# Optimization experiments

Hardware: AMD Instinct MI355X
Metric: run time of the kernel (lower is better)

Reference implementation:

```python
import jax, jax.numpy as jnp
import numpy as np

N, C, K = 262144, 64, 27  # active voxels, channels, 3^3 kernel offsets


def setup_inputs() -> dict:
    key = jax.random.key(0)
    k1, k2, k3, k4, k5, k6, k7 = jax.random.split(key, 7)
    features = jax.random.normal(k1, (N, C), dtype=jnp.float32)
    # kernel map: for each offset k and output voxel n, index of contributing input voxel
    nbr_idx = jax.random.randint(k2, (K, N), 0, N, dtype=jnp.int32)
    mask = jax.random.uniform(k3, (K, N)) < 0.4
    scale = 1.0 / np.sqrt(K * C)
    w1 = jax.random.normal(k4, (K, C, C), dtype=jnp.float32) * scale
    b1 = jax.random.normal(k5, (C,), dtype=jnp.float32) * 0.01
    w2 = jax.random.normal(k6, (K, C, C), dtype=jnp.float32) * scale
    b2 = jax.random.normal(k7, (C,), dtype=jnp.float32) * 0.01
    return dict(features=features, nbr_idx=nbr_idx, mask=mask,
                w1=w1, b1=b1, w2=w2, b2=b2)


def _sparse_conv(feat, nbr_idx, mask, W, b):
    """Explicit-GEMM sparse conv: per kernel offset, gather -> GEMM -> accumulate."""
    def step(acc, xs):
        idx, m, Wk = xs                                  # [N], [N], [C, C]
        g = feat[idx] * m[:, None].astype(feat.dtype)    # gather + zero invalid: [N, C]
        return acc + g @ Wk, None
    acc, _ = jax.lax.scan(step, jnp.zeros_like(feat), (nbr_idx, mask, W))
    return acc + b


def reference(features, nbr_idx, mask, w1, b1, w2, b2):
    h = _sparse_conv(features, nbr_idx, mask, w1, b1)
    h = _sparse_conv(h, nbr_idx, mask, w2, b2)
    return h + features  # residual add of input feature tensor
```

## Files before the change

kernel.cpp:

```cpp
#include <hip/hip_runtime.h>
#include <stdint.h>

#define N_VOX 262144
#define CCH 64
#define KOFF 27

typedef short v8s __attribute__((ext_vector_type(8)));
typedef float v4f __attribute__((ext_vector_type(4)));

#define GLD16(gp, lp) __builtin_amdgcn_global_load_lds(                     \
    (const __attribute__((address_space(1))) void*)(gp),                    \
    (__attribute__((address_space(3))) void*)(lp), 16, 0, 0)

__device__ __forceinline__ unsigned short f2bf(float f) {
  unsigned u = __float_as_uint(f);
  u += 0x7fff + ((u >> 16) & 1);
  return (unsigned short)(u >> 16);
}

__global__ void prep_flag_k(const unsigned* __restrict__ m, int* __restrict__ flag) {
  if (threadIdx.x == 0) {
    int wordlike = 1;
    for (int i = 0; i < 256; ++i) {
      unsigned v = m[i];
      if (v > 1u && v != 0x3f800000u) { wordlike = 0; break; }
    }
    *flag = wordlike ? 0 : 2;
  }
}

__global__ void prep_mask_k(const void* __restrict__ m, const int* __restrict__ flag,
                            unsigned char* __restrict__ mb, int n) {
  int f = *flag;
  for (int i = blockIdx.x * blockDim.x + threadIdx.x; i < n; i += gridDim.x * blockDim.x) {
    unsigned char v;
    if (f == 2) v = (((const unsigned char*)m)[i] != 0);
    else        v = (((const unsigned*)m)[i] != 0u);
    mb[i] = v;
  }
}

__global__ void prep_feat_k(const float* __restrict__ src, unsigned short* __restrict__ dst, int n8) {
  int i = blockIdx.x * blockDim.x + threadIdx.x;
  if (i >= n8) return;
  const float4* s4 = (const float4*)src;
  float4 a = s4[i * 2], b = s4[i * 2 + 1];
  v8s v;
  v[0] = (short)f2bf(a.x); v[1] = (short)f2bf(a.y);
  v[2] = (short)f2bf(a.z); v[3] = (short)f2bf(a.w);
  v[4] = (short)f2bf(b.x); v[5] = (short)f2bf(b.y);
  v[6] = (short)f2bf(b.z); v[7] = (short)f2bf(b.w);
  ((v8s*)dst)[i] = v;
}

__global__ void prep_w_k(const float* __restrict__ w, unsigned short* __restrict__ wt) {
  int i = blockIdx.x * blockDim.x + threadIdx.x;
  if (i >= KOFF * CCH * CCH) return;
  int e = i & 7, lane = (i >> 3) & 63, ch = (i >> 9) & 7, k = i >> 12;
  int ct = ch >> 1, half = ch & 1;
  int col = ct * 16 + (lane & 15);
  int kk = half * 32 + ((lane >> 4) << 3) + e;
  wt[i] = f2bf(w[(k << 12) + (kk << 6) + col]);
}

__device__ __forceinline__ void conv_body(
    int k, bool last, char* slot, const v8s* __restrict__ Wc, char* WnB,
    const char* __restrict__ src8B, const char* __restrict__ wfgB,
    const int* __restrict__ nbr, const unsigned char* __restrict__ mb,
    int lane, int g, int tid16, int r0, int r1,
    int& jz0, int& jz1, int& mz0, int& mz1,
    int jd0, int jd1, int md0, int md1,
    v4f (&acc)[2][4])
{
  asm volatile("s_waitcnt vmcnt(4)" ::: "memory");
  v8s a0 = *(const v8s*)(slot + lane * 16);
  v8s a1 = *(const v8s*)(slot + 1024 + lane * 16);
  v8s a2 = *(const v8s*)(slot + 2048 + lane * 16);
  v8s a3 = *(const v8s*)(slot + 3072 + lane * 16);
  if (!mz0) { a0 = (v8s){}; a1 = (v8s){}; }
  if (!mz1) { a2 = (v8s){}; a3 = (v8s){}; }
  asm volatile("s_waitcnt lgkmcnt(0)" ::: "memory");
  __builtin_amdgcn_sched_barrier(0);

  if (!last) {
    GLD16(wfgB + (size_t)(k + 1) * 8192 + tid16, WnB);
    long e0 = (long)(md0 ? jd0 : 0) * 128 + g * 16;
    long e1 = (long)(md1 ? jd1 : 0) * 128 + g * 16;
    GLD16(src8B + e0,      slot);
    GLD16(src8B + e0 + 64, slot + 1024);
    GLD16(src8B + e1,      slot + 2048);
    GLD16(src8B + e1 + 64, slot + 3072);
    const int kj = (k + 2 < KOFF) ? k + 2 : KOFF - 1;
    jz0 = nbr[kj * N_VOX + r0]; jz1 = nbr[kj * N_VOX + r1];
    mz0 = mb[kj * N_VOX + r0];  mz1 = mb[kj * N_VOX + r1];
  }

#pragma unroll
  for (int ct = 0; ct < 4; ++ct) {
    v8s blo = Wc[ct * 128 + lane];
    v8s bhi = Wc[ct * 128 + 64 + lane];
    acc[0][ct] = __builtin_amdgcn_mfma_f32_16x16x32_bf16(a0, blo, acc[0][ct], 0, 0, 0);
    acc[0][ct] = __builtin_amdgcn_mfma_f32_16x16x32_bf16(a1, bhi, acc[0][ct], 0, 0, 0);
    acc[1][ct] = __builtin_amdgcn_mfma_f32_16x16x32_bf16(a2, blo, acc[1][ct], 0, 0, 0);
    acc[1][ct] = __builtin_amdgcn_mfma_f32_16x16x32_bf16(a3, bhi, acc[1][ct], 0, 0, 0);
  }

  if (!last) {
    asm volatile("s_waitcnt vmcnt(8)" ::: "memory");
    __builtin_amdgcn_s_barrier();
  }
}

template <int LAYER>
__global__ __launch_bounds__(512, 4)
void conv_layer_k(const char* __restrict__ src8B, const int* __restrict__ nbr,
                  const unsigned char* __restrict__ mb,
                  const char* __restrict__ wfgB, const float* __restrict__ bias,
                  const float* __restrict__ resid, void* __restrict__ outp) {
  __shared__ char ldsW[2][8192];
  __shared__ char ldsA[8][4096];
  const int tid = threadIdx.x;
  const int lane = tid & 63;
  const int wv = tid >> 6;
  const int l15 = lane & 15;
  const int g = lane >> 4;
  const int tid16 = tid * 16;
  const int rowbase = blockIdx.x * 256 + wv * 32;
  const int r0 = rowbase + l15;
  const int r1 = r0 + 16;
  char* slot = ldsA[wv];

  int jE0 = nbr[r0], jE1 = nbr[r1];
  int mE0 = mb[r0],  mE1 = mb[r1];
  {
    long e0 = (long)(mE0 ? jE0 : 0) * 128 + g * 16;
    long e1 = (long)(mE1 ? jE1 : 0) * 128 + g * 16;
    GLD16(src8B + e0,      slot);
    GLD16(src8B + e0 + 64, slot + 1024);
    GLD16(src8B + e1,      slot + 2048);
    GLD16(src8B + e1 + 64, slot + 3072);
  }
  GLD16(wfgB + tid16, (char*)ldsW[0] + wv * 1024);
  int jO0 = nbr[N_VOX + r0], jO1 = nbr[N_VOX + r1];
  int mO0 = mb[N_VOX + r0],  mO1 = mb[N_VOX + r1];
  asm volatile("s_waitcnt vmcnt(0)" ::: "memory");
  __builtin_amdgcn_s_barrier();

  v4f acc[2][4] = {};

#pragma unroll 1
  for (int k = 0; k < KOFF - 1; k += 2) {
    conv_body(k, false, slot, (const v8s*)ldsW[0], (char*)ldsW[1] + wv * 1024,
              src8B, wfgB, nbr, mb, lane, g, tid16, r0, r1,
              jE0, jE1, mE0, mE1, jO0, jO1, mO0, mO1, acc);
    conv_body(k + 1, false, slot, (const v8s*)ldsW[1], (char*)ldsW[0] + wv * 1024,
              src8B, wfgB, nbr, mb, lane, g, tid16, r0, r1,
              jO0, jO1, mO0, mO1, jE0, jE1, mE0, mE1, acc);
  }
  conv_body(KOFF - 1, true, slot, (const v8s*)ldsW[0], (char*)ldsW[1] + wv * 1024,
            src8B, wfgB, nbr, mb, lane, g, tid16, r0, r1,
            jE0, jE1, mE0, mE1, jO0, jO1, mO0, mO1, acc);

  float bv[4];
#pragma unroll
  for (int ct = 0; ct < 4; ++ct) bv[ct] = bias[ct * 16 + l15];

#pragma unroll
  for (int rt = 0; rt < 2; ++rt) {
    int row0 = rowbase + rt * 16 + g * 4;
#pragma unroll
    for (int ct = 0; ct < 4; ++ct) {
      int col = ct * 16 + l15;
#pragma unroll
      for (int i = 0; i < 4; ++i) {
        float v = acc[rt][ct][i] + bv[ct];
        int o = (row0 + i) * CCH + col;
        if (LAYER == 1) ((unsigned short*)outp)[o] = f2bf(v);
        else            ((float*)outp)[o] = v + resid[o];
      }
    }
  }
}

extern "C" void kernel_launch(void* const* d_in, const int* in_sizes, int n_in,
                              void* d_out, int out_size, void* d_ws, size_t ws_size,
                              hipStream_t stream) {
  const float* feat = (const float*)d_in[0];
  const int* nbr    = (const int*)d_in[1];
  const void* mask  = d_in[2];
  const float* w1   = (const float*)d_in[3];
  const float* b1   = (const float*)d_in[4];
  const float* w2   = (const float*)d_in[5];
  const float* b2   = (const float*)d_in[6];

  char* ws = (char*)d_ws;
  unsigned short* featb = (unsigned short*)ws;
  unsigned short* hb    = (unsigned short*)(ws + 33554432);
  unsigned char*  maskb = (unsigned char*)(ws + 67108864);
  unsigned short* wf1   = (unsigned short*)(ws + 74186752);
  unsigned short* wf2   = (unsigned short*)(ws + 74407936);
  int*            flag  = (int*)(ws + 74629120);

  prep_flag_k<<<1, 64, 0, stream>>>((const unsigned*)mask, flag);
  prep_mask_k<<<4096, 256, 0, stream>>>(mask, flag, maskb, KOFF * N_VOX);
  prep_feat_k<<<8192, 256, 0, stream>>>(feat, featb, N_VOX * CCH / 8);
  prep_w_k<<<432, 256, 0, stream>>>(w1, wf1);
  prep_w_k<<<432, 256, 0, stream>>>(w2, wf2);

  conv_layer_k<1><<<1024, 512, 0, stream>>>((const char*)featb, nbr, maskb,
                                            (const char*)wf1, b1, nullptr, (void*)hb);
  conv_layer_k<2><<<1024, 512, 0, stream>>>((const char*)hb, nbr, maskb,
                                            (const char*)wf2, b2, feat, (void*)d_out);
}
```

Measured before the change: 250.3 us.

## Double-buffer gathered rows, stage weights through registers, halve block size

```diff
diff --git a/kernel.cpp b/kernel.cpp
--- a/kernel.cpp
+++ b/kernel.cpp
@@ -64,41 +64,47 @@
 }
 
 __device__ __forceinline__ void conv_body(
-    int k, bool last, char* slot, const v8s* __restrict__ Wc, char* WnB,
-    const char* __restrict__ src8B, const char* __restrict__ wfgB,
+    int k, bool last, char* Wb, char* slotC, char* slotN,
+    const char* __restrict__ src8B, const v8s* __restrict__ wfg,
     const int* __restrict__ nbr, const unsigned char* __restrict__ mb,
-    int lane, int g, int tid16, int r0, int r1,
-    int& jz0, int& jz1, int& mz0, int& mz1,
-    int jd0, int jd1, int md0, int md1,
+    int lane, int wv, int g, int l15, int rme,
+    int& iN, int& mN, int& mc0, int& mc1,
     v4f (&acc)[2][4])
 {
-  asm volatile("s_waitcnt vmcnt(4)" ::: "memory");
-  v8s a0 = *(const v8s*)(slot + lane * 16);
-  v8s a1 = *(const v8s*)(slot + 1024 + lane * 16);
-  v8s a2 = *(const v8s*)(slot + 2048 + lane * 16);
-  v8s a3 = *(const v8s*)(slot + 3072 + lane * 16);
-  if (!mz0) { a0 = (v8s){}; a1 = (v8s){}; }
-  if (!mz1) { a2 = (v8s){}; a3 = (v8s){}; }
-  asm volatile("s_waitcnt lgkmcnt(0)" ::: "memory");
-  __builtin_amdgcn_sched_barrier(0);
-
+  asm volatile("s_waitcnt vmcnt(2)" ::: "memory");
+  v8s w0, w1;
+  int v0 = 0, v1 = 0;
   if (!last) {
-    GLD16(wfgB + (size_t)(k + 1) * 8192 + tid16, WnB);
-    long e0 = (long)(md0 ? jd0 : 0) * 128 + g * 16;
-    long e1 = (long)(md1 ? jd1 : 0) * 128 + g * 16;
-    GLD16(src8B + e0,      slot);
-    GLD16(src8B + e0 + 64, slot + 1024);
-    GLD16(src8B + e1,      slot + 2048);
-    GLD16(src8B + e1 + 64, slot + 3072);
+    w0 = wfg[(k + 1) * 512 + wv * 128 + lane];
+    w1 = wfg[(k + 1) * 512 + wv * 128 + 64 + lane];
+    asm volatile("s_waitcnt vmcnt(2)" ::: "memory");
+    int j0 = __shfl(iN, l15, 64);
+    int j1 = __shfl(iN, 16 + l15, 64);
+    v0 = __shfl(mN, l15, 64);
+    v1 = __shfl(mN, 16 + l15, 64);
+    long e0 = (long)(v0 ? j0 : 0) * 128 + g * 16;
+    long e1 = (long)(v1 ? j1 : 0) * 128 + g * 16;
+    GLD16(src8B + e0,      slotN);
+    GLD16(src8B + e0 + 64, slotN + 1024);
+    GLD16(src8B + e1,      slotN + 2048);
+    GLD16(src8B + e1 + 64, slotN + 3072);
     const int kj = (k + 2 < KOFF) ? k + 2 : KOFF - 1;
-    jz0 = nbr[kj * N_VOX + r0]; jz1 = nbr[kj * N_VOX + r1];
-    mz0 = mb[kj * N_VOX + r0];  mz1 = mb[kj * N_VOX + r1];
-  }
+    iN = nbr[kj * N_VOX + rme];
+    mN = mb[kj * N_VOX + rme];
+  }
+
+  v8s a0 = *(const v8s*)(slotC + lane * 16);
+  v8s a1 = *(const v8s*)(slotC + 1024 + lane * 16);
+  v8s a2 = *(const v8s*)(slotC + 2048 + lane * 16);
+  v8s a3 = *(const v8s*)(slotC + 3072 + lane * 16);
+  if (!mc0) { a0 = (v8s){}; a1 = (v8s){}; }
+  if (!mc1) { a2 = (v8s){}; a3 = (v8s){}; }
+  mc0 = v0; mc1 = v1;
 
 #pragma unroll
   for (int ct = 0; ct < 4; ++ct) {
-    v8s blo = Wc[ct * 128 + lane];
-    v8s bhi = Wc[ct * 128 + 64 + lane];
+    v8s blo = *(const v8s*)(Wb + (ct * 2) * 1024 + lane * 16);
+    v8s bhi = *(const v8s*)(Wb + (ct * 2 + 1) * 1024 + lane * 16);
     acc[0][ct] = __builtin_amdgcn_mfma_f32_16x16x32_bf16(a0, blo, acc[0][ct], 0, 0, 0);
     acc[0][ct] = __builtin_amdgcn_mfma_f32_16x16x32_bf16(a1, bhi, acc[0][ct], 0, 0, 0);
     acc[1][ct] = __builtin_amdgcn_mfma_f32_16x16x32_bf16(a2, blo, acc[1][ct], 0, 0, 0);
@@ -106,60 +112,70 @@
   }
 
   if (!last) {
-    asm volatile("s_waitcnt vmcnt(8)" ::: "memory");
+    asm volatile("s_waitcnt lgkmcnt(0)" ::: "memory");
+    __builtin_amdgcn_sched_barrier(0);
     __builtin_amdgcn_s_barrier();
+    *(v8s*)(Wb + (wv * 128 + lane) * 16) = w0;
+    *(v8s*)(Wb + (wv * 128 + 64 + lane) * 16) = w1;
+    asm volatile("s_waitcnt lgkmcnt(0)" ::: "memory");
+    __builtin_amdgcn_sched_barrier(0);
+    __builtin_amdgcn_s_barrier();
   }
 }
 
 template <int LAYER>
-__global__ __launch_bounds__(512, 4)
+__global__ __launch_bounds__(256, 4)
 void conv_layer_k(const char* __restrict__ src8B, const int* __restrict__ nbr,
                   const unsigned char* __restrict__ mb,
-                  const char* __restrict__ wfgB, const float* __restrict__ bias,
+                  const v8s* __restrict__ wfg, const float* __restrict__ bias,
                   const float* __restrict__ resid, void* __restrict__ outp) {
-  __shared__ char ldsW[2][8192];
-  __shared__ char ldsA[8][4096];
+  __shared__ char ldsW[8192];
+  __shared__ char ldsA[4][2][4096];
   const int tid = threadIdx.x;
   const int lane = tid & 63;
   const int wv = tid >> 6;
   const int l15 = lane & 15;
   const int g = lane >> 4;
-  const int tid16 = tid * 16;
-  const int rowbase = blockIdx.x * 256 + wv * 32;
-  const int r0 = rowbase + l15;
-  const int r1 = r0 + 16;
-  char* slot = ldsA[wv];
-
-  int jE0 = nbr[r0], jE1 = nbr[r1];
-  int mE0 = mb[r0],  mE1 = mb[r1];
+  const int rowbase = blockIdx.x * 128 + wv * 32;
+  const int rme = rowbase + (lane & 31);
+  char* slotE = ldsA[wv][0];
+  char* slotO = ldsA[wv][1];
+
+  int iN = nbr[rme];
+  int mN = mb[rme];
+  v8s w0 = wfg[wv * 128 + lane];
+  v8s w1 = wfg[wv * 128 + 64 + lane];
+  int mc0 = __shfl(mN, l15, 64);
+  int mc1 = __shfl(mN, 16 + l15, 64);
   {
-    long e0 = (long)(mE0 ? jE0 : 0) * 128 + g * 16;
-    long e1 = (long)(mE1 ? jE1 : 0) * 128 + g * 16;
-    GLD16(src8B + e0,      slot);
-    GLD16(src8B + e0 + 64, slot + 1024);
-    GLD16(src8B + e1,      slot + 2048);
-    GLD16(src8B + e1 + 64, slot + 3072);
-  }
-  GLD16(wfgB + tid16, (char*)ldsW[0] + wv * 1024);
-  int jO0 = nbr[N_VOX + r0], jO1 = nbr[N_VOX + r1];
-  int mO0 = mb[N_VOX + r0],  mO1 = mb[N_VOX + r1];
-  asm volatile("s_waitcnt vmcnt(0)" ::: "memory");
+    int j0 = __shfl(iN, l15, 64);
+    int j1 = __shfl(iN, 16 + l15, 64);
+    long e0 = (long)(mc0 ? j0 : 0) * 128 + g * 16;
+    long e1 = (long)(mc1 ? j1 : 0) * 128 + g * 16;
+    GLD16(src8B + e0,      slotE);
+    GLD16(src8B + e0 + 64, slotE + 1024);
+    GLD16(src8B + e1,      slotE + 2048);
+    GLD16(src8B + e1 + 64, slotE + 3072);
+  }
+  iN = nbr[N_VOX + rme];
+  mN = mb[N_VOX + rme];
+  *(v8s*)(ldsW + (wv * 128 + lane) * 16) = w0;
+  *(v8s*)(ldsW + (wv * 128 + 64 + lane) * 16) = w1;
+  asm volatile("s_waitcnt lgkmcnt(0)" ::: "memory");
+  __builtin_amdgcn_sched_barrier(0);
   __builtin_amdgcn_s_barrier();
 
   v4f acc[2][4] = {};
 
 #pragma unroll 1
   for (int k = 0; k < KOFF - 1; k += 2) {
-    conv_body(k, false, slot, (const v8s*)ldsW[0], (char*)ldsW[1] + wv * 1024,
-              src8B, wfgB, nbr, mb, lane, g, tid16, r0, r1,
-              jE0, jE1, mE0, mE1, jO0, jO1, mO0, mO1, acc);
-    conv_body(k + 1, false, slot, (const v8s*)ldsW[1], (char*)ldsW[0] + wv * 1024,
-              src8B, wfgB, nbr, mb, lane, g, tid16, r0, r1,
-              jO0, jO1, mO0, mO1, jE0, jE1, mE0, mE1, acc);
-  }
-  conv_body(KOFF - 1, true, slot, (const v8s*)ldsW[0], (char*)ldsW[1] + wv * 1024,
-            src8B, wfgB, nbr, mb, lane, g, tid16, r0, r1,
-            jE0, jE1, mE0, mE1, jO0, jO1, mO0, mO1, acc);
+    conv_body(k,     false, ldsW, slotE, slotO, src8B, wfg, nbr, mb,
+              lane, wv, g, l15, rme, iN, mN, mc0, mc1, acc);
+    conv_body(k + 1, false, ldsW, slotO, slotE, src8B, wfg, nbr, mb,
+              lane, wv, g, l15, rme, iN, mN, mc0, mc1, acc);
+  }
+  conv_body(KOFF - 1, true, ldsW, slotE, slotO, src8B, wfg, nbr, mb,
+            lane, wv, g, l15, rme, iN, mN, mc0, mc1, acc);
 
   float bv[4];
 #pragma unroll
@@ -207,8 +223,8 @@
   prep_w_k<<<432, 256, 0, stream>>>(w1, wf1);
   prep_w_k<<<432, 256, 0, stream>>>(w2, wf2);
 
-  conv_layer_k<1><<<1024, 512, 0, stream>>>((const char*)featb, nbr, maskb,
-                                            (const char*)wf1, b1, nullptr, (void*)hb);
-  conv_layer_k<2><<<1024, 512, 0, stream>>>((const char*)hb, nbr, maskb,
-                                            (const char*)wf2, b2, feat, (void*)d_out);
-}
+  conv_layer_k<1><<<2048, 256, 0, stream>>>((const char*)featb, nbr, maskb,
+                                            (const v8s*)wf1, b1, nullptr, (void*)hb);
+  conv_layer_k<2><<<2048, 256, 0, stream>>>((const char*)hb, nbr, maskb,
+                                            (const v8s*)wf2, b2, feat, (void*)d_out);
+}
```

After: 243.6 us. 1.03x faster.
